# Performance work log

Hardware: AMD Instinct MI355X
Metric: run time of the kernel (lower is better)

The kernel has to match this reference:

```python
import jax, jax.numpy as jnp
import numpy as np

N_HEADS = 16
D_EMBED = 1024
D_CROSS = 768
D_HEAD = D_EMBED // N_HEADS


def setup_inputs() -> dict:
    key = jax.random.key(0)
    ks = jax.random.split(key, 10)
    B, SQ, SKV = 8, 4096, 77
    s_e = 1.0 / np.sqrt(D_EMBED)
    s_c = 1.0 / np.sqrt(D_CROSS)
    return {
        "x": jax.random.normal(ks[0], (B, SQ, D_EMBED), jnp.float32),
        "y": jax.random.normal(ks[1], (B, SKV, D_CROSS), jnp.float32),
        "wq": jax.random.normal(ks[2], (D_EMBED, D_EMBED), jnp.float32) * s_e,
        "bq": jnp.zeros((D_EMBED,), jnp.float32),
        "wk": jax.random.normal(ks[3], (D_CROSS, D_EMBED), jnp.float32) * s_c,
        "bk": jnp.zeros((D_EMBED,), jnp.float32),
        "wv": jax.random.normal(ks[4], (D_CROSS, D_EMBED), jnp.float32) * s_c,
        "bv": jnp.zeros((D_EMBED,), jnp.float32),
        "wo": jax.random.normal(ks[5], (D_EMBED, D_EMBED), jnp.float32) * s_e,
        "bo": jnp.zeros((D_EMBED,), jnp.float32),
    }


def reference(x, y, wq, bq, wk, bk, wv, bv, wo, bo):
    B, SQ, _ = x.shape
    SKV = y.shape[1]
    # projections
    q = (x @ wq + bq).reshape(B, SQ, N_HEADS, D_HEAD)
    k = (y @ wk + bk).reshape(B, SKV, N_HEADS, D_HEAD)
    v = (y @ wv + bv).reshape(B, SKV, N_HEADS, D_HEAD)
    # scaled dot-product attention, heads as axis h
    scores = jnp.einsum("bqhd,bkhd->bhqk", q, k) / jnp.sqrt(
        jnp.asarray(D_HEAD, x.dtype))
    attn = jax.nn.softmax(scores, axis=-1)
    out = jnp.einsum("bhqk,bkhd->bqhd", attn, v).reshape(B, SQ, D_EMBED)
    return out @ wo + bo
```

## Files before the change

### kernel.cpp

```cpp
#include <hip/hip_runtime.h>
#include <stdint.h>

#define NH 16
#define DH 64
#define DE 1024
#define DC 768
#define NB 8
#define SQL 4096
#define SKV 77
#define QCH 512

typedef __attribute__((ext_vector_type(8))) short s16x8;
typedef __attribute__((ext_vector_type(4))) float f32x4;

__device__ inline ushort f2b(float f) {
    union { float f; uint32_t u; } v; v.f = f;
    uint32_t u = v.u;
    uint32_t r = (u + 0x7FFFu + ((u >> 16) & 1u)) >> 16;
    return (ushort)r;
}

__device__ inline void gload_lds16(const void* g, void* l) {
    __builtin_amdgcn_global_load_lds(
        (const __attribute__((address_space(1))) void*)g,
        (__attribute__((address_space(3))) void*)l, 16, 0, 0);
}

__global__ void cvt_f32_bf16(const float* __restrict__ in, ushort* __restrict__ out,
                             long long n) {
    long long i = ((long long)blockIdx.x * 256 + threadIdx.x) * 8;
    if (i >= n) return;
    float4 a = *(const float4*)(in + i);
    float4 b = *(const float4*)(in + i + 4);
    ushort4 r0 = make_ushort4(f2b(a.x), f2b(a.y), f2b(a.z), f2b(a.w));
    ushort4 r1 = make_ushort4(f2b(b.x), f2b(b.y), f2b(b.z), f2b(b.w));
    *(ushort4*)(out + i) = r0;
    *(ushort4*)(out + i + 4) = r1;
}

__global__ void transpose_cvt(const float* __restrict__ in, ushort* __restrict__ out,
                              int K, int N) {
    __shared__ float tile[32][33];
    const int tx = threadIdx.x, ty = threadIdx.y;
    const int bn = blockIdx.x * 32, bk = blockIdx.y * 32;
#pragma unroll
    for (int i = 0; i < 4; ++i)
        tile[ty + i * 8][tx] = in[(size_t)(bk + ty + i * 8) * N + bn + tx];
    __syncthreads();
#pragma unroll
    for (int i = 0; i < 4; ++i)
        out[(size_t)(bn + ty + i * 8) * K + bk + tx] = f2b(tile[tx][ty + i * 8]);
}

__global__ void pack_bias(const float* __restrict__ bk, const float* __restrict__ bv,
                          float* __restrict__ bkv) {
    int i = blockIdx.x * 256 + threadIdx.x;
    if (i < 2048) bkv[i] = (i < 1024) ? bk[i] : bv[i - 1024];
}

template <int OUTBF>
__global__ __launch_bounds__(256, 2)
void gemm_bt(const ushort* __restrict__ A, const ushort* __restrict__ Bt,
             const float* __restrict__ bias, void* __restrict__ Cout,
             int M, int N, int K, int Mvalid, float scale, int nby) {
    __shared__ ushort As[128][32];
    __shared__ ushort Bs[128][32];
    const int tid = threadIdx.x;
    const int lane = tid & 63, wid = tid >> 6;
    const int wr = wid >> 1, wc = wid & 1;
    const int l = blockIdx.x;
    const int q8 = gridDim.x >> 3;
    const int rm = (l & 7) * q8 + (l >> 3);
    const int row0 = (rm / nby) * 128, col0 = (rm % nby) * 128;

    const int srow = tid >> 2;
    const int sk = (tid & 3) * 8;
    const ushort* Ag = A + (size_t)(row0 + srow) * K + sk;
    const ushort* Bg = Bt + (size_t)(col0 + srow) * K + sk;
    ushort* Asl = &As[srow][sk];
    ushort* Asl2 = &As[srow + 64][sk];
    ushort* Bsl = &Bs[srow][sk];
    ushort* Bsl2 = &Bs[srow + 64][sk];
    const size_t rstep = (size_t)64 * K;

    f32x4 acc[4][4] = {};
    const int mrow = wr * 64 + (lane & 15);
    const int ncol = wc * 64 + (lane & 15);
    const int kfr = (lane >> 4) * 8;

    const int nk = K >> 5;
    for (int kt = 0; kt < nk; ++kt) {
        gload_lds16(Ag, Asl);
        gload_lds16(Ag + rstep, Asl2);
        gload_lds16(Bg, Bsl);
        gload_lds16(Bg + rstep, Bsl2);
        Ag += 32; Bg += 32;
        __syncthreads();
        s16x8 af[4], bfr[4];
#pragma unroll
        for (int m = 0; m < 4; ++m)
            af[m] = *(const s16x8*)&As[mrow + m * 16][kfr];
#pragma unroll
        for (int n = 0; n < 4; ++n)
            bfr[n] = *(const s16x8*)&Bs[ncol + n * 16][kfr];
#pragma unroll
        for (int m = 0; m < 4; ++m)
#pragma unroll
            for (int n = 0; n < 4; ++n)
                acc[m][n] = __builtin_amdgcn_mfma_f32_16x16x32_bf16(
                    af[m], bfr[n], acc[m][n], 0, 0, 0);
        __syncthreads();
    }

    const int r0 = row0 + wr * 64 + ((lane >> 4) << 2);
    const int c0 = col0 + wc * 64 + (lane & 15);
#pragma unroll
    for (int n = 0; n < 4; ++n) {
        const int c = c0 + n * 16;
        const float bv = bias[c];
#pragma unroll
        for (int m = 0; m < 4; ++m) {
#pragma unroll
            for (int r = 0; r < 4; ++r) {
                const int row = r0 + m * 16 + r;
                if (row < Mvalid) {
                    float v = acc[m][n][r] + bv;
                    if (OUTBF)
                        ((ushort*)Cout)[(size_t)row * N + c] = f2b(v * scale);
                    else
                        ((float*)Cout)[(size_t)row * N + c] = v;
                }
            }
        }
    }
}

__global__ __launch_bounds__(256, 4)
void attn(const ushort* __restrict__ q, const ushort* __restrict__ kv,
          ushort* __restrict__ o) {
    __shared__ ushort Ks[80][72];
    __shared__ ushort Vt[64][104];
    __shared__ ushort Ps[64][104];

    const int qc = blockIdx.x;
    const int bh = blockIdx.y;
    const int b = bh >> 4, h = bh & 15;
    const int tid = threadIdx.x, lane = tid & 63, wid = tid >> 6;
    const int g = lane >> 4, qi = lane & 15;
    const int kfr = g * 8;
    const int kvb = g * 4;

    const ushort* kbase = kv + (size_t)b * SKV * 2048 + h * 64;
    const ushort* vbase = kbase + 1024;

    for (int i = tid; i < 64 * 27; i += 256) {
        int d = i / 27, c = 77 + i % 27;
        Vt[d][c] = 0;
    }
    {
        int row = tid >> 3;
        const int cs = (tid & 7) * 8;
#pragma unroll
        for (int pass = 0; pass < 3; ++pass, row += 32)
            if (row < 80) {
                const int sr = row < SKV ? row : SKV - 1;
                *(uint4*)&Ks[row][cs] = *(const uint4*)(kbase + (size_t)sr * 2048 + cs);
            }
    }
    for (int t = tid; t < SKV * 8; t += 256) {
        const int s = t >> 3, d8 = (t & 7) * 8;
        ushort tmp[8];
        *(uint4*)tmp = *(const uint4*)(vbase + (size_t)s * 2048 + d8);
#pragma unroll
        for (int j = 0; j < 8; ++j) Vt[d8 + j][s] = tmp[j];
    }
    __syncthreads();

    const size_t qrow0 = (size_t)b * SQL + (size_t)qc * QCH;
    const ushort* qb = q + (qrow0 + wid * 16 + qi) * DE + h * 64 + kfr;

    for (int it = 0; it < QCH / 64; ++it) {
        const ushort* qp = qb + (size_t)it * 64 * DE;
        s16x8 aq0 = *(const s16x8*)qp;
        s16x8 aq1 = *(const s16x8*)(qp + 32);

        f32x4 accs[5] = {};
#pragma unroll
        for (int n = 0; n < 5; ++n) {
            s16x8 k0 = *(const s16x8*)&Ks[n * 16 + qi][kfr];
            s16x8 k1 = *(const s16x8*)&Ks[n * 16 + qi][kfr + 32];
            accs[n] = __builtin_amdgcn_mfma_f32_16x16x32_bf16(k0, aq0, accs[n], 0, 0, 0);
            accs[n] = __builtin_amdgcn_mfma_f32_16x16x32_bf16(k1, aq1, accs[n], 0, 0, 0);
        }

        float ev[5][4];
        float m = -1e30f;
#pragma unroll
        for (int n = 0; n < 5; ++n)
#pragma unroll
            for (int r = 0; r < 4; ++r) {
                float v = accs[n][r];
                v = (n * 16 + kvb + r < SKV) ? v : -1e30f;
                ev[n][r] = v;
                m = fmaxf(m, v);
            }
        m = fmaxf(m, __shfl_xor(m, 16));
        m = fmaxf(m, __shfl_xor(m, 32));
        float s = 0.f;
#pragma unroll
        for (int n = 0; n < 5; ++n)
#pragma unroll
            for (int r = 0; r < 4; ++r) {
                float e = __expf(ev[n][r] - m);
                ev[n][r] = e;
                s += e;
            }
        s += __shfl_xor(s, 16);
        s += __shfl_xor(s, 32);
        const float inv = 1.f / s;

        {
            ushort* pr = &Ps[wid * 16 + qi][0];
#pragma unroll
            for (int n = 0; n < 5; ++n) {
#pragma unroll
                for (int rp = 0; rp < 4; rp += 2) {
                    uint32_t u = (uint32_t)f2b(ev[n][rp] * inv) |
                                 ((uint32_t)f2b(ev[n][rp + 1] * inv) << 16);
                    *(uint32_t*)&pr[n * 16 + kvb + rp] = u;
                }
            }
            *(uint32_t*)&pr[80 + kvb] = 0;
            *(uint32_t*)&pr[80 + kvb + 2] = 0;
        }

        f32x4 acco[4] = {};
#pragma unroll
        for (int kk = 0; kk < 3; ++kk) {
            s16x8 pa = *(const s16x8*)&Ps[wid * 16 + qi][kk * 32 + kfr];
#pragma unroll
            for (int n2 = 0; n2 < 4; ++n2) {
                s16x8 vb = *(const s16x8*)&Vt[n2 * 16 + qi][kk * 32 + kfr];
                acco[n2] = __builtin_amdgcn_mfma_f32_16x16x32_bf16(pa, vb, acco[n2], 0, 0, 0);
            }
        }
        const size_t orow = qrow0 + it * 64 + wid * 16 + kvb;
#pragma unroll
        for (int n2 = 0; n2 < 4; ++n2)
#pragma unroll
            for (int r = 0; r < 4; ++r)
                o[(orow + r) * DE + h * 64 + n2 * 16 + qi] = f2b(acco[n2][r]);
    }
}

extern "C" void kernel_launch(void* const* d_in, const int* in_sizes, int n_in,
                              void* d_out, int out_size, void* d_ws, size_t ws_size,
                              hipStream_t stream) {
    const float* x = (const float*)d_in[0];
    const float* y = (const float*)d_in[1];
    const float* wq = (const float*)d_in[2];
    const float* bq = (const float*)d_in[3];
    const float* wk = (const float*)d_in[4];
    const float* bk = (const float*)d_in[5];
    const float* wv = (const float*)d_in[6];
    const float* bv = (const float*)d_in[7];
    const float* wo = (const float*)d_in[8];
    const float* bo = (const float*)d_in[9];
    float* out = (float*)d_out;

    char* ws = (char*)d_ws;
    ushort* x16 = (ushort*)ws;  ws += (size_t)32768 * 1024 * 2;
    ushort* q16 = (ushort*)ws;  ws += (size_t)32768 * 1024 * 2;
    ushort* y16 = (ushort*)ws;  ws += (size_t)640 * 768 * 2;
    ushort* kv16 = (ushort*)ws; ws += (size_t)640 * 2048 * 2;
    ushort* wqt = (ushort*)ws;  ws += (size_t)1024 * 1024 * 2;
    ushort* wkvt = (ushort*)ws; ws += (size_t)2048 * 768 * 2;
    ushort* wot = (ushort*)ws;  ws += (size_t)1024 * 1024 * 2;
    float* bkv = (float*)ws;    ws += 2048 * 4;

    cvt_f32_bf16<<<16384, 256, 0, stream>>>(x, x16, 33554432LL);
    cvt_f32_bf16<<<231, 256, 0, stream>>>(y, y16, 473088LL);
    transpose_cvt<<<dim3(32, 32), dim3(32, 8), 0, stream>>>(wq, wqt, 1024, 1024);
    transpose_cvt<<<dim3(32, 24), dim3(32, 8), 0, stream>>>(wk, wkvt, 768, 1024);
    transpose_cvt<<<dim3(32, 24), dim3(32, 8), 0, stream>>>(wv, wkvt + (size_t)1024 * 768, 768, 1024);
    transpose_cvt<<<dim3(32, 32), dim3(32, 8), 0, stream>>>(wo, wot, 1024, 1024);
    pack_bias<<<8, 256, 0, stream>>>(bk, bv, bkv);
    gemm_bt<1><<<80, 256, 0, stream>>>(y16, wkvt, bkv, kv16, 640, 2048, 768, 616, 1.0f, 16);
    gemm_bt<1><<<2048, 256, 0, stream>>>(x16, wqt, bq, q16, 32768, 1024, 1024, 32768, 0.125f, 8);
    attn<<<dim3(8, 128), 256, 0, stream>>>(q16, kv16, x16);
    gemm_bt<0><<<2048, 256, 0, stream>>>(x16, wot, bo, out, 32768, 1024, 1024, 32768, 1.0f, 8);
}
```

Before: 525.8 us.

## Use 256x256-tile double-buffered GEMM kernel for Q and output projections

Adds a new 512-thread GEMM kernel that computes 256x256 output tiles. It stages operands into double-buffered LDS with direct global-to-LDS loads, XOR-swizzles the LDS layout, and raises wave priority around the MFMA blocks. The kernel replaces the previous 128-tile gemm_bt for the two large 32768x1024x1024 projections, aiming for more data reuse per tile and better overlap of loads with compute. The larger tile uses 128 KB of LDS and many accumulator registers per thread, which limits occupancy. It also assumes M and N divide evenly by 256 and has no bounds checks.

```diff
diff --git a/kernel.cpp b/kernel.cpp
--- a/kernel.cpp
+++ b/kernel.cpp
@@ -135,6 +135,127 @@
     }
 }
 
+template <int OUTBF>
+__global__ __launch_bounds__(512, 2)
+void gemm256(const ushort* __restrict__ A, const ushort* __restrict__ Bt,
+             const float* __restrict__ bias, void* __restrict__ Cout,
+             int N, int K, float scale, int nby) {
+    __shared__ ushort lds[2][2][256 * 64];
+    const int tid = threadIdx.x, lane = tid & 63;
+    const int wid = tid >> 6, wr = wid >> 2, wc = wid & 3;
+    const int l = blockIdx.x, q8 = gridDim.x >> 3;
+    const int rm = (l & 7) * q8 + (l >> 3);
+    const int row0 = (rm / nby) * 256, col0 = (rm % nby) * 256;
+
+    const int sr = tid >> 3;
+    const int scx = ((tid & 7) ^ (sr & 7)) * 8;
+    const ushort* Agp = A + (size_t)(row0 + sr) * K + scx;
+    const ushort* Bgp = Bt + (size_t)(col0 + sr) * K + scx;
+
+    const int nt = K >> 6;
+
+    auto STAGE = [&](int t, int b) {
+#pragma unroll
+        for (int j = 0; j < 4; ++j)
+            gload_lds16(Agp + (size_t)j * 64 * K + t * 64,
+                        &lds[b][0][(j * 512 + tid) * 8]);
+#pragma unroll
+        for (int j = 0; j < 4; ++j)
+            gload_lds16(Bgp + (size_t)j * 64 * K + t * 64,
+                        &lds[b][1][(j * 512 + tid) * 8]);
+    };
+
+    const int fr = lane & 15, fk = lane >> 4;
+    const int xk0 = ((fk) ^ (fr & 7)) * 16;
+    const int xk1 = ((fk + 4) ^ (fr & 7)) * 16;
+
+    f32x4 acc[8][4] = {};
+
+    STAGE(0, 0);
+    STAGE(1, 1);
+    asm volatile("s_waitcnt vmcnt(8)" ::: "memory");
+    __builtin_amdgcn_s_barrier();
+    __builtin_amdgcn_sched_barrier(0);
+
+    for (int t = 0; t < nt; ++t) {
+        const char* Ab = (const char*)&lds[t & 1][0][0];
+        const char* Bb = (const char*)&lds[t & 1][1][0];
+        s16x8 afrag[4][2], bfrag[4][2];
+#pragma unroll
+        for (int n = 0; n < 4; ++n) {
+            const int br = (wc * 64 + n * 16 + fr) * 128;
+            bfrag[n][0] = *(const s16x8*)(Bb + br + xk0);
+            bfrag[n][1] = *(const s16x8*)(Bb + br + xk1);
+        }
+#pragma unroll
+        for (int m = 0; m < 4; ++m) {
+            const int ar = (wr * 128 + m * 16 + fr) * 128;
+            afrag[m][0] = *(const s16x8*)(Ab + ar + xk0);
+            afrag[m][1] = *(const s16x8*)(Ab + ar + xk1);
+        }
+        __builtin_amdgcn_s_setprio(1);
+#pragma unroll
+        for (int m = 0; m < 4; ++m)
+#pragma unroll
+            for (int n = 0; n < 4; ++n) {
+                acc[m][n] = __builtin_amdgcn_mfma_f32_16x16x32_bf16(
+                    afrag[m][0], bfrag[n][0], acc[m][n], 0, 0, 0);
+                acc[m][n] = __builtin_amdgcn_mfma_f32_16x16x32_bf16(
+                    afrag[m][1], bfrag[n][1], acc[m][n], 0, 0, 0);
+            }
+        __builtin_amdgcn_s_setprio(0);
+#pragma unroll
+        for (int m = 0; m < 4; ++m) {
+            const int ar = (wr * 128 + 64 + m * 16 + fr) * 128;
+            afrag[m][0] = *(const s16x8*)(Ab + ar + xk0);
+            afrag[m][1] = *(const s16x8*)(Ab + ar + xk1);
+        }
+        __builtin_amdgcn_s_setprio(1);
+#pragma unroll
+        for (int m = 0; m < 4; ++m)
+#pragma unroll
+            for (int n = 0; n < 4; ++n) {
+                acc[4 + m][n] = __builtin_amdgcn_mfma_f32_16x16x32_bf16(
+                    afrag[m][0], bfrag[n][0], acc[4 + m][n], 0, 0, 0);
+                acc[4 + m][n] = __builtin_amdgcn_mfma_f32_16x16x32_bf16(
+                    afrag[m][1], bfrag[n][1], acc[4 + m][n], 0, 0, 0);
+            }
+        __builtin_amdgcn_s_setprio(0);
+        __builtin_amdgcn_sched_barrier(0);
+        __builtin_amdgcn_s_barrier();
+        __builtin_amdgcn_sched_barrier(0);
+        if (t + 2 < nt) {
+            STAGE(t + 2, t & 1);
+            asm volatile("s_waitcnt vmcnt(8)" ::: "memory");
+        } else {
+            asm volatile("s_waitcnt vmcnt(0)" ::: "memory");
+        }
+        __builtin_amdgcn_sched_barrier(0);
+        __builtin_amdgcn_s_barrier();
+        __builtin_amdgcn_sched_barrier(0);
+    }
+
+    const int r00 = row0 + wr * 128 + fk * 4;
+    const int c00 = col0 + wc * 64 + fr;
+#pragma unroll
+    for (int n = 0; n < 4; ++n) {
+        const int c = c00 + n * 16;
+        const float bv = bias[c];
+#pragma unroll
+        for (int m = 0; m < 8; ++m) {
+#pragma unroll
+            for (int r = 0; r < 4; ++r) {
+                const int row = r00 + m * 16 + r;
+                const float v = (acc[m][n][r] + bv) * scale;
+                if (OUTBF)
+                    ((ushort*)Cout)[(size_t)row * N + c] = f2b(v);
+                else
+                    ((float*)Cout)[(size_t)row * N + c] = v;
+            }
+        }
+    }
+}
+
 __global__ __launch_bounds__(256, 4)
 void attn(const ushort* __restrict__ q, const ushort* __restrict__ kv,
           ushort* __restrict__ o) {
@@ -163,8 +284,8 @@
 #pragma unroll
         for (int pass = 0; pass < 3; ++pass, row += 32)
             if (row < 80) {
-                const int sr = row < SKV ? row : SKV - 1;
-                *(uint4*)&Ks[row][cs] = *(const uint4*)(kbase + (size_t)sr * 2048 + cs);
+                const int srw = row < SKV ? row : SKV - 1;
+                *(uint4*)&Ks[row][cs] = *(const uint4*)(kbase + (size_t)srw * 2048 + cs);
             }
     }
     for (int t = tid; t < SKV * 8; t += 256) {
@@ -286,7 +407,7 @@
     transpose_cvt<<<dim3(32, 32), dim3(32, 8), 0, stream>>>(wo, wot, 1024, 1024);
     pack_bias<<<8, 256, 0, stream>>>(bk, bv, bkv);
     gemm_bt<1><<<80, 256, 0, stream>>>(y16, wkvt, bkv, kv16, 640, 2048, 768, 616, 1.0f, 16);
-    gemm_bt<1><<<2048, 256, 0, stream>>>(x16, wqt, bq, q16, 32768, 1024, 1024, 32768, 0.125f, 8);
+    gemm256<1><<<512, 512, 0, stream>>>(x16, wqt, bq, q16, 1024, 1024, 0.125f, 4);
     attn<<<dim3(8, 128), 256, 0, stream>>>(q16, kv16, x16);
-    gemm_bt<0><<<2048, 256, 0, stream>>>(x16, wot, bo, out, 32768, 1024, 1024, 32768, 1.0f, 8);
-}
+    gemm256<0><<<512, 512, 0, stream>>>(x16, wot, bo, out, 1024, 1024, 1.0f, 4);
+}
```

Result: faster. 498.1 us (-5.3%).
